# Kernel optimization log

Measured on AMD Instinct MI355X. Metric: run time of the kernel, lower is better.

Reference implementation:

```python
import jax, jax.numpy as jnp
import numpy as np

EPS_NORM = 1e-6  # MVLayerNorm epsilon


def _build_cayley():
    # Cl(3,0): blades as bitmasks, ordered by (grade, bitmask):
    # [1, e1, e2, e3, e12, e13, e23, e123]
    n = 3
    order = sorted(range(1 << n), key=lambda b: (bin(b).count('1'), b))
    idx = {b: i for i, b in enumerate(order)}
    C = np.zeros((8, 8, 8), dtype=np.float32)
    for a in range(8):
        for b in range(8):
            # sign from reordering basis vectors (Euclidean metric: e_i^2 = +1)
            swaps, ash = 0, a >> 1
            while ash:
                swaps += bin(ash & b).count('1')
                ash >>= 1
            C[idx[a], idx[a ^ b], idx[b]] = -1.0 if swaps % 2 else 1.0
    return C

_CAYLEY_NP = _build_cayley()
CAYLEY = jnp.asarray(_CAYLEY_NP)
# metric of each blade: scalar part of blade*blade -> [1,1,1,1,-1,-1,-1,-1]
METRIC = jnp.asarray(np.array([_CAYLEY_NP[i, 0, i] for i in range(8)], dtype=np.float32))
# blade -> grade subspace index, subspace dims [1,3,3,1]
BLADE2SUB = np.array([0, 1, 1, 1, 2, 2, 2, 3])


def mv_linear(x, w, b):
    # x: (B, in, 8); w: (out, in, 4); b: (out,) added to scalar blade only
    wb = w[:, :, BLADE2SUB]                      # (out, in, 8) per-blade weight
    y = jnp.einsum('bmi,nmi->bni', x, wb)        # (B, out, 8)
    return y.at[..., 0].add(b)


def mv_layernorm(x, a):
    # quadratic form per channel: q = sum_i g_i * x_i^2, shape (B, C, 1)
    q = jnp.einsum('bci,i,bci->bc', x, METRIC, x)[..., None]
    norm = (q * q + 1e-16) ** 0.25               # smooth sqrt(|q|)
    norm = norm.mean(axis=1, keepdims=True) + EPS_NORM  # (B, 1, 1)
    return a[None, :, None] * x / norm


def setup_inputs() -> dict:
    key = jax.random.key(0)
    ks = jax.random.split(key, 8)
    N, C_IN, C_HID, NSUB = 4096, 512, 512, 4
    s = 1.0 / np.sqrt(C_IN)
    return {
        'x': jax.random.normal(ks[0], (N, C_IN, 8), jnp.float32),
        'w1': jax.random.normal(ks[1], (C_HID, C_IN, NSUB), jnp.float32) * s,
        'b1': jax.random.normal(ks[2], (C_HID,), jnp.float32) * 0.02,
        'w2': jax.random.normal(ks[3], (C_HID, C_IN, NSUB), jnp.float32) * s,
        'b2': jax.random.normal(ks[4], (C_HID,), jnp.float32) * 0.02,
        'w3': jax.random.normal(ks[5], (C_IN, C_HID, NSUB), jnp.float32) * s,
        'b3': jax.random.normal(ks[6], (C_IN,), jnp.float32) * 0.02,
        'a_norm': jax.random.normal(ks[7], (C_IN,), jnp.float32) * 0.1 + 1.0,
    }


def reference(x, w1, b1, w2, b2, w3, b3, a_norm):
    x_l = mv_linear(x, w1, b1)                       # (N, hid, 8)
    x_r = mv_linear(x, w2, b2)                       # (N, hid, 8)
    gp = jnp.einsum('bni,ijk,bnk->bnj', x_l, CAYLEY, x_r)  # sparse Cayley product
    y = mv_linear(gp, w3, b3)                        # (N, in, 8)
    return mv_layernorm(y, a_norm)
```

## Files before the change

kernel.cpp:

```cpp
#include <hip/hip_runtime.h>
#include <hip/hip_bf16.h>
#include <cstdint>
#include <cstddef>

typedef __bf16 bf16;
typedef __bf16 bf16x2_t __attribute__((ext_vector_type(2)));
typedef __bf16 bf16x4_t __attribute__((ext_vector_type(4)));
typedef __bf16 bf16x8_t __attribute__((ext_vector_type(8)));
typedef float  f32x2_t  __attribute__((ext_vector_type(2)));
typedef float  f32x4_t  __attribute__((ext_vector_type(4)));
typedef unsigned int u32x4_t __attribute__((ext_vector_type(4)));

#define NTOK 4096
#define CH   512
#define SLICE (NTOK*CH)
#define WSLICE (CH*CH)

#define AS1 __attribute__((address_space(1)))
#define AS3 __attribute__((address_space(3)))

__device__ __forceinline__ void gl_lds16(const void* g, void* l) {
    __builtin_amdgcn_global_load_lds((const AS1 unsigned int*)g,
                                     (AS3 unsigned int*)l, 16, 0, 0);
}

__global__ __launch_bounds__(256) void k_convert_x(const float* __restrict__ x,
                                                   bf16* __restrict__ xb) {
    int p = blockIdx.x * 256 + threadIdx.x;
    const f32x4_t* x4 = (const f32x4_t*)x;
    f32x4_t v0 = x4[2*p];
    f32x4_t v1 = x4[2*p+1];
    xb[0*SLICE + p] = (bf16)v0.x;
    xb[1*SLICE + p] = (bf16)v0.y;
    xb[2*SLICE + p] = (bf16)v0.z;
    xb[3*SLICE + p] = (bf16)v0.w;
    xb[4*SLICE + p] = (bf16)v1.x;
    xb[5*SLICE + p] = (bf16)v1.y;
    xb[6*SLICE + p] = (bf16)v1.z;
    xb[7*SLICE + p] = (bf16)v1.w;
}

__global__ __launch_bounds__(256) void k_convert_w(const float* __restrict__ w1,
                                                   const float* __restrict__ w2,
                                                   const float* __restrict__ w3,
                                                   bf16* __restrict__ w1b,
                                                   bf16* __restrict__ w2b,
                                                   bf16* __restrict__ w3b) {
    int p = blockIdx.x * 256 + threadIdx.x;
    const float* w = (blockIdx.y == 0) ? w1 : (blockIdx.y == 1) ? w2 : w3;
    bf16* wb       = (blockIdx.y == 0) ? w1b : (blockIdx.y == 1) ? w2b : w3b;
    f32x4_t v = ((const f32x4_t*)w)[p];
    wb[0*WSLICE + p] = (bf16)v.x;
    wb[1*WSLICE + p] = (bf16)v.y;
    wb[2*WSLICE + p] = (bf16)v.z;
    wb[3*WSLICE + p] = (bf16)v.w;
}

template<int DUAL>
__global__ __launch_bounds__(256, 2) void k_gemm(const bf16* __restrict__ Abase,
                                                 const bf16* __restrict__ W1base,
                                                 const bf16* __restrict__ W2base,
                                                 bf16* __restrict__ O1base,
                                                 bf16* __restrict__ O2base) {
    const int blade = blockIdx.z;
    const int sub = (blade == 0) ? 0 : (blade < 4) ? 1 : (blade < 7) ? 2 : 3;
    const bf16* A  = Abase + (size_t)blade * SLICE;
    const bf16* B1 = W1base + (size_t)sub * WSLICE;
    const bf16* B2 = W2base + (size_t)sub * WSLICE;
    const int tm = blockIdx.x * 128, tn = blockIdx.y * 128;

    __shared__ __align__(1024) bf16 lsA[128 * 64];
    __shared__ __align__(1024) bf16 lsB1[128 * 64];
    __shared__ __align__(1024) bf16 lsB2[DUAL ? 128 * 64 : 64];
    char* lsAc  = (char*)lsA;
    char* lsB1c = (char*)lsB1;
    char* lsB2c = (char*)lsB2;

    const int t = threadIdx.x, lane = t & 63, wid = t >> 6;
    const int waveM = (wid >> 1) * 64, waveN = (wid & 1) * 64;

    const int srow = wid * 32 + (lane >> 3);
    const int sswz = ((lane & 7) ^ (srow & 7)) * 8;
    const bf16* Ag  = A  + (size_t)(tm + srow) * CH + sswz;
    const bf16* B1g = B1 + (size_t)(tn + srow) * CH + sswz;
    const bf16* B2g = B2 + (size_t)(tn + srow) * CH + sswz;
    const int ldsq = wid * 4096;

    const int xorv  = (lane & 7) << 4;
    const int kbase = (lane >> 4) * 16;

    f32x4_t accL[4][4] = {};
    f32x4_t accR[4][4] = {};

    #pragma unroll 1
    for (int kt = 0; kt < 8; ++kt) {
        __syncthreads();
        const int k0 = kt * 64;
        #pragma unroll
        for (int q = 0; q < 4; ++q) {
            gl_lds16(Ag  + (size_t)q * 8 * CH + k0, lsAc  + ldsq + q * 1024);
            gl_lds16(B1g + (size_t)q * 8 * CH + k0, lsB1c + ldsq + q * 1024);
            if constexpr (DUAL)
                gl_lds16(B2g + (size_t)q * 8 * CH + k0, lsB2c + ldsq + q * 1024);
        }
        __syncthreads();
        #pragma unroll
        for (int kk = 0; kk < 2; ++kk) {
            const int koff = kk * 64 + kbase;
            bf16x8_t af[4], b1v[4], b2v[4];
            #pragma unroll
            for (int mf = 0; mf < 4; ++mf) {
                int row = waveM + mf * 16 + (lane & 15);
                af[mf] = *(const bf16x8_t*)(lsAc + row * 128 + (koff ^ xorv));
            }
            #pragma unroll
            for (int nf = 0; nf < 4; ++nf) {
                int row = waveN + nf * 16 + (lane & 15);
                b1v[nf] = *(const bf16x8_t*)(lsB1c + row * 128 + (koff ^ xorv));
                if constexpr (DUAL)
                    b2v[nf] = *(const bf16x8_t*)(lsB2c + row * 128 + (koff ^ xorv));
            }
            #pragma unroll
            for (int mf = 0; mf < 4; ++mf)
                #pragma unroll
                for (int nf = 0; nf < 4; ++nf) {
                    accL[mf][nf] = __builtin_amdgcn_mfma_f32_16x16x32_bf16(
                        af[mf], b1v[nf], accL[mf][nf], 0, 0, 0);
                    if constexpr (DUAL)
                        accR[mf][nf] = __builtin_amdgcn_mfma_f32_16x16x32_bf16(
                            af[mf], b2v[nf], accR[mf][nf], 0, 0, 0);
                }
        }
    }

    const int orow0 = tm + waveM + (lane >> 4) * 4;
    const int ocol  = tn + waveN + (lane & 15);
    bf16* O1 = O1base + (size_t)blade * SLICE;
    #pragma unroll
    for (int mf = 0; mf < 4; ++mf)
        #pragma unroll
        for (int r = 0; r < 4; ++r) {
            size_t rowoff = (size_t)(orow0 + mf * 16 + r) * CH;
            #pragma unroll
            for (int nf = 0; nf < 4; ++nf)
                O1[rowoff + ocol + nf * 16] = (bf16)accL[mf][nf][r];
        }
    if constexpr (DUAL) {
        bf16* O2 = O2base + (size_t)blade * SLICE;
        #pragma unroll
        for (int mf = 0; mf < 4; ++mf)
            #pragma unroll
            for (int r = 0; r < 4; ++r) {
                size_t rowoff = (size_t)(orow0 + mf * 16 + r) * CH;
                #pragma unroll
                for (int nf = 0; nf < 4; ++nf)
                    O2[rowoff + ocol + nf * 16] = (bf16)accR[mf][nf][r];
            }
    }
}

__global__ __launch_bounds__(256) void k_gp(const bf16* __restrict__ xl,
                                            const bf16* __restrict__ xr,
                                            const float* __restrict__ b1,
                                            const float* __restrict__ b2,
                                            bf16* __restrict__ gp) {
    int p = (blockIdx.x * 256 + threadIdx.x) * 4;
    float l[8][4], r[8][4], g[8][4];
    #pragma unroll
    for (int i = 0; i < 8; ++i) {
        bf16x4_t lv = *(const bf16x4_t*)(xl + (size_t)i * SLICE + p);
        bf16x4_t rv = *(const bf16x4_t*)(xr + (size_t)i * SLICE + p);
        #pragma unroll
        for (int v = 0; v < 4; ++v) { l[i][v] = (float)lv[v]; r[i][v] = (float)rv[v]; g[i][v] = 0.f; }
    }
    int n0 = p & (CH - 1);
    f32x4_t b1v = *(const f32x4_t*)(b1 + n0);
    f32x4_t b2v = *(const f32x4_t*)(b2 + n0);
    #pragma unroll
    for (int v = 0; v < 4; ++v) { l[0][v] += b1v[v]; r[0][v] += b2v[v]; }

    const int IDX[8] = {0, 1, 2, 4, 3, 5, 6, 7};
    #pragma unroll
    for (int a = 0; a < 8; ++a) {
        #pragma unroll
        for (int b = 0; b < 8; ++b) {
            int e = ((((a >> 1) ^ (a >> 2)) & b) & 1) ^ (((a >> 2) & (b >> 1)) & 1);
            int j = IDX[a ^ b], ia = IDX[a], ib = IDX[b];
            #pragma unroll
            for (int v = 0; v < 4; ++v)
                g[j][v] += e ? (-l[ia][v] * r[ib][v]) : (l[ia][v] * r[ib][v]);
        }
    }
    #pragma unroll
    for (int i = 0; i < 8; ++i) {
        bf16x4_t gv;
        #pragma unroll
        for (int v = 0; v < 4; ++v) gv[v] = (bf16)g[i][v];
        *(bf16x4_t*)(gp + (size_t)i * SLICE + p) = gv;
    }
}

__global__ __launch_bounds__(256) void k_ln(const bf16* __restrict__ y,
                                            const float* __restrict__ b3,
                                            const float* __restrict__ an,
                                            float* __restrict__ out) {
    int b = blockIdx.x, t = threadIdx.x;
    int c0 = t * 2;
    size_t base = (size_t)b * CH + c0;
    float yv[2][8];
    #pragma unroll
    for (int i = 0; i < 8; ++i) {
        bf16x2_t v = *(const bf16x2_t*)(y + (size_t)i * SLICE + base);
        yv[0][i] = (float)v[0];
        yv[1][i] = (float)v[1];
    }
    f32x2_t b3v = *(const f32x2_t*)(b3 + c0);
    float nsum = 0.f;
    #pragma unroll
    for (int h = 0; h < 2; ++h) {
        yv[h][0] += b3v[h];
        float q = yv[h][0]*yv[h][0] + yv[h][1]*yv[h][1] + yv[h][2]*yv[h][2] + yv[h][3]*yv[h][3]
                - yv[h][4]*yv[h][4] - yv[h][5]*yv[h][5] - yv[h][6]*yv[h][6] - yv[h][7]*yv[h][7];
        nsum += sqrtf(sqrtf(q * q + 1e-16f));
    }
    #pragma unroll
    for (int off = 32; off; off >>= 1) nsum += __shfl_xor(nsum, off);
    __shared__ float red[4];
    if ((t & 63) == 0) red[t >> 6] = nsum;
    __syncthreads();
    float denom = (red[0] + red[1] + red[2] + red[3]) * (1.f / 512.f) + 1e-6f;
    float inv = 1.f / denom;
    f32x2_t anv = *(const f32x2_t*)(an + c0);
    float out16[16];
    #pragma unroll
    for (int h = 0; h < 2; ++h) {
        float s = anv[h] * inv;
        #pragma unroll
        for (int i = 0; i < 8; ++i) out16[h * 8 + i] = yv[h][i] * s;
    }
    size_t base8 = base * 8;
    #pragma unroll
    for (int j = 0; j < 4; ++j)
        *(f32x4_t*)(out + base8 + j * 4) = *(f32x4_t*)(out16 + j * 4);
}

extern "C" void kernel_launch(void* const* d_in, const int* in_sizes, int n_in,
                              void* d_out, int out_size, void* d_ws, size_t ws_size,
                              hipStream_t stream) {
    (void)in_sizes; (void)n_in; (void)out_size; (void)ws_size;
    const float* x  = (const float*)d_in[0];
    const float* w1 = (const float*)d_in[1];
    const float* b1 = (const float*)d_in[2];
    const float* w2 = (const float*)d_in[3];
    const float* b2 = (const float*)d_in[4];
    const float* w3 = (const float*)d_in[5];
    const float* b3 = (const float*)d_in[6];
    const float* an = (const float*)d_in[7];

    char* ws = (char*)d_ws;
    bf16*  xb  = (bf16*)(ws);
    bf16*  xl  = (bf16*)(ws + 33554432);
    bf16*  xr  = (bf16*)(ws + 67108864);
    bf16*  yb  = (bf16*)(ws + 33554432);
    bf16*  w1b = (bf16*)(ws + 100663296);
    bf16*  w2b = (bf16*)(ws + 102760448);
    bf16*  w3b = (bf16*)(ws + 104857600);

    k_convert_x<<<SLICE / 256, 256, 0, stream>>>(x, xb);
    dim3 gw(WSLICE / 256, 3);
    k_convert_w<<<gw, 256, 0, stream>>>(w1, w2, w3, w1b, w2b, w3b);

    dim3 gg(NTOK / 128, CH / 128, 8);
    k_gemm<1><<<gg, 256, 0, stream>>>(xb, w1b, w2b, xl, xr);
    k_gp<<<SLICE / 4 / 256, 256, 0, stream>>>(xl, xr, b1, b2, xb );
    k_gemm<0><<<gg, 256, 0, stream>>>(xb, w3b, w3b, yb, yb);
    k_ln<<<NTOK, 256, 0, stream>>>(yb, b3, an, (float*)d_out);
}
```

Before: 244.6 us.

## Double-buffer LDS and enlarge GEMM tiles with 512-thread blocks

Splits the templated GEMM into two kernels: a dual GEMM for the two input projections and a single GEMM for the output projection. Both now use 512-thread blocks with larger output tiles (256x128 and 256x256) and double-buffered LDS. The next K tile is prefetched through global_load_lds while the current one is multiplied, which halves the barriers per iteration. MFMA sections are wrapped in s_setprio. The aim is to hide global-load latency and raise data reuse per LDS byte. In exchange, each block now needs 128KB of LDS, which likely limits occupancy to one block per CU, and the GEMM3 grid shrinks to a single wave of blocks.

```diff
diff --git a/kernel.cpp b/kernel.cpp
--- a/kernel.cpp
+++ b/kernel.cpp
@@ -9,7 +9,6 @@
 typedef __bf16 bf16x8_t __attribute__((ext_vector_type(8)));
 typedef float  f32x2_t  __attribute__((ext_vector_type(2)));
 typedef float  f32x4_t  __attribute__((ext_vector_type(4)));
-typedef unsigned int u32x4_t __attribute__((ext_vector_type(4)));
 
 #define NTOK 4096
 #define CH   512
@@ -56,107 +55,208 @@
     wb[3*WSLICE + p] = (bf16)v.w;
 }
 
-template<int DUAL>
-__global__ __launch_bounds__(256, 2) void k_gemm(const bf16* __restrict__ Abase,
-                                                 const bf16* __restrict__ W1base,
-                                                 const bf16* __restrict__ W2base,
-                                                 bf16* __restrict__ O1base,
-                                                 bf16* __restrict__ O2base) {
+__global__ __launch_bounds__(512, 2) void k_gemm12(const bf16* __restrict__ xb,
+                                                   const bf16* __restrict__ w1b,
+                                                   const bf16* __restrict__ w2b,
+                                                   bf16* __restrict__ xl,
+                                                   bf16* __restrict__ xr) {
     const int blade = blockIdx.z;
     const int sub = (blade == 0) ? 0 : (blade < 4) ? 1 : (blade < 7) ? 2 : 3;
-    const bf16* A  = Abase + (size_t)blade * SLICE;
-    const bf16* B1 = W1base + (size_t)sub * WSLICE;
-    const bf16* B2 = W2base + (size_t)sub * WSLICE;
-    const int tm = blockIdx.x * 128, tn = blockIdx.y * 128;
-
-    __shared__ __align__(1024) bf16 lsA[128 * 64];
-    __shared__ __align__(1024) bf16 lsB1[128 * 64];
-    __shared__ __align__(1024) bf16 lsB2[DUAL ? 128 * 64 : 64];
-    char* lsAc  = (char*)lsA;
-    char* lsB1c = (char*)lsB1;
-    char* lsB2c = (char*)lsB2;
+    const bf16* A  = xb  + (size_t)blade * SLICE;
+    const bf16* B1 = w1b + (size_t)sub * WSLICE;
+    const bf16* B2 = w2b + (size_t)sub * WSLICE;
+    const int tm = blockIdx.x * 256, tn = blockIdx.y * 128;
+
+    __shared__ __align__(1024) bf16 lsA[2][256 * 64];
+    __shared__ __align__(1024) bf16 lsB1[2][128 * 64];
+    __shared__ __align__(1024) bf16 lsB2[2][128 * 64];
 
     const int t = threadIdx.x, lane = t & 63, wid = t >> 6;
-    const int waveM = (wid >> 1) * 64, waveN = (wid & 1) * 64;
-
-    const int srow = wid * 32 + (lane >> 3);
-    const int sswz = ((lane & 7) ^ (srow & 7)) * 8;
+    const int waveM = (wid >> 2) * 128, waveN = (wid & 3) * 32;
+
+    const int srow = t >> 3;
+    const int sswz = ((t & 7) ^ (srow & 7)) * 8;
     const bf16* Ag  = A  + (size_t)(tm + srow) * CH + sswz;
     const bf16* B1g = B1 + (size_t)(tn + srow) * CH + sswz;
     const bf16* B2g = B2 + (size_t)(tn + srow) * CH + sswz;
-    const int ldsq = wid * 4096;
+    const int wbase = wid * 1024;
 
     const int xorv  = (lane & 7) << 4;
     const int kbase = (lane >> 4) * 16;
 
-    f32x4_t accL[4][4] = {};
-    f32x4_t accR[4][4] = {};
-
-    #pragma unroll 1
+    f32x4_t accL[8][2] = {};
+    f32x4_t accR[8][2] = {};
+
+    {
+        char* la  = (char*)lsA[0]  + wbase;
+        char* lb1 = (char*)lsB1[0] + wbase;
+        char* lb2 = (char*)lsB2[0] + wbase;
+        #pragma unroll
+        for (int q = 0; q < 4; ++q)
+            gl_lds16(Ag + (size_t)q * 64 * CH, la + q * 8192);
+        #pragma unroll
+        for (int q = 0; q < 2; ++q) {
+            gl_lds16(B1g + (size_t)q * 64 * CH, lb1 + q * 8192);
+            gl_lds16(B2g + (size_t)q * 64 * CH, lb2 + q * 8192);
+        }
+    }
+
+    #pragma unroll 2
     for (int kt = 0; kt < 8; ++kt) {
+        const int cur = kt & 1;
         __syncthreads();
-        const int k0 = kt * 64;
-        #pragma unroll
-        for (int q = 0; q < 4; ++q) {
-            gl_lds16(Ag  + (size_t)q * 8 * CH + k0, lsAc  + ldsq + q * 1024);
-            gl_lds16(B1g + (size_t)q * 8 * CH + k0, lsB1c + ldsq + q * 1024);
-            if constexpr (DUAL)
-                gl_lds16(B2g + (size_t)q * 8 * CH + k0, lsB2c + ldsq + q * 1024);
-        }
-        __syncthreads();
+        if (kt < 7) {
+            const int k0 = (kt + 1) * 64;
+            char* la  = (char*)lsA[cur ^ 1]  + wbase;
+            char* lb1 = (char*)lsB1[cur ^ 1] + wbase;
+            char* lb2 = (char*)lsB2[cur ^ 1] + wbase;
+            #pragma unroll
+            for (int q = 0; q < 4; ++q)
+                gl_lds16(Ag + (size_t)q * 64 * CH + k0, la + q * 8192);
+            #pragma unroll
+            for (int q = 0; q < 2; ++q) {
+                gl_lds16(B1g + (size_t)q * 64 * CH + k0, lb1 + q * 8192);
+                gl_lds16(B2g + (size_t)q * 64 * CH + k0, lb2 + q * 8192);
+            }
+        }
+        const char* ca  = (const char*)lsA[cur];
+        const char* cb1 = (const char*)lsB1[cur];
+        const char* cb2 = (const char*)lsB2[cur];
         #pragma unroll
         for (int kk = 0; kk < 2; ++kk) {
             const int koff = kk * 64 + kbase;
-            bf16x8_t af[4], b1v[4], b2v[4];
-            #pragma unroll
-            for (int mf = 0; mf < 4; ++mf) {
+            bf16x8_t af[8], b1f[2], b2f[2];
+            #pragma unroll
+            for (int mf = 0; mf < 8; ++mf) {
                 int row = waveM + mf * 16 + (lane & 15);
-                af[mf] = *(const bf16x8_t*)(lsAc + row * 128 + (koff ^ xorv));
+                af[mf] = *(const bf16x8_t*)(ca + row * 128 + (koff ^ xorv));
+            }
+            #pragma unroll
+            for (int nf = 0; nf < 2; ++nf) {
+                int row = waveN + nf * 16 + (lane & 15);
+                b1f[nf] = *(const bf16x8_t*)(cb1 + row * 128 + (koff ^ xorv));
+                b2f[nf] = *(const bf16x8_t*)(cb2 + row * 128 + (koff ^ xorv));
+            }
+            __builtin_amdgcn_s_setprio(1);
+            #pragma unroll
+            for (int mf = 0; mf < 8; ++mf)
+                #pragma unroll
+                for (int nf = 0; nf < 2; ++nf) {
+                    accL[mf][nf] = __builtin_amdgcn_mfma_f32_16x16x32_bf16(
+                        af[mf], b1f[nf], accL[mf][nf], 0, 0, 0);
+                    accR[mf][nf] = __builtin_amdgcn_mfma_f32_16x16x32_bf16(
+                        af[mf], b2f[nf], accR[mf][nf], 0, 0, 0);
+                }
+            __builtin_amdgcn_s_setprio(0);
+        }
+    }
+
+    bf16* O1 = xl + (size_t)blade * SLICE;
+    bf16* O2 = xr + (size_t)blade * SLICE;
+    const int orow0 = tm + waveM + (lane >> 4) * 4;
+    const int ocol  = tn + waveN + (lane & 15);
+    #pragma unroll
+    for (int mf = 0; mf < 8; ++mf)
+        #pragma unroll
+        for (int r = 0; r < 4; ++r) {
+            size_t rowoff = (size_t)(orow0 + mf * 16 + r) * CH;
+            #pragma unroll
+            for (int nf = 0; nf < 2; ++nf) {
+                O1[rowoff + ocol + nf * 16] = (bf16)accL[mf][nf][r];
+                O2[rowoff + ocol + nf * 16] = (bf16)accR[mf][nf][r];
+            }
+        }
+}
+
+__global__ __launch_bounds__(512, 2) void k_gemm3(const bf16* __restrict__ gp,
+                                                  const bf16* __restrict__ w3b,
+                                                  bf16* __restrict__ yb) {
+    const int blade = blockIdx.z;
+    const int sub = (blade == 0) ? 0 : (blade < 4) ? 1 : (blade < 7) ? 2 : 3;
+    const bf16* A = gp  + (size_t)blade * SLICE;
+    const bf16* B = w3b + (size_t)sub * WSLICE;
+    const int tm = blockIdx.x * 256, tn = blockIdx.y * 256;
+
+    __shared__ __align__(1024) bf16 lsA[2][256 * 64];
+    __shared__ __align__(1024) bf16 lsB[2][256 * 64];
+
+    const int t = threadIdx.x, lane = t & 63, wid = t >> 6;
+    const int waveM = (wid >> 2) * 128, waveN = (wid & 3) * 64;
+
+    const int srow = t >> 3;
+    const int sswz = ((t & 7) ^ (srow & 7)) * 8;
+    const bf16* Ag = A + (size_t)(tm + srow) * CH + sswz;
+    const bf16* Bg = B + (size_t)(tn + srow) * CH + sswz;
+    const int wbase = wid * 1024;
+
+    const int xorv  = (lane & 7) << 4;
+    const int kbase = (lane >> 4) * 16;
+
+    f32x4_t acc[8][4] = {};
+
+    {
+        char* la = (char*)lsA[0] + wbase;
+        char* lb = (char*)lsB[0] + wbase;
+        #pragma unroll
+        for (int q = 0; q < 4; ++q) {
+            gl_lds16(Ag + (size_t)q * 64 * CH, la + q * 8192);
+            gl_lds16(Bg + (size_t)q * 64 * CH, lb + q * 8192);
+        }
+    }
+
+    #pragma unroll 2
+    for (int kt = 0; kt < 8; ++kt) {
+        const int cur = kt & 1;
+        __syncthreads();
+        if (kt < 7) {
+            const int k0 = (kt + 1) * 64;
+            char* la = (char*)lsA[cur ^ 1] + wbase;
+            char* lb = (char*)lsB[cur ^ 1] + wbase;
+            #pragma unroll
+            for (int q = 0; q < 4; ++q) {
+                gl_lds16(Ag + (size_t)q * 64 * CH + k0, la + q * 8192);
+                gl_lds16(Bg + (size_t)q * 64 * CH + k0, lb + q * 8192);
+            }
+        }
+        const char* ca = (const char*)lsA[cur];
+        const char* cb = (const char*)lsB[cur];
+        #pragma unroll
+        for (int kk = 0; kk < 2; ++kk) {
+            const int koff = kk * 64 + kbase;
+            bf16x8_t af[8], bf[4];
+            #pragma unroll
+            for (int mf = 0; mf < 8; ++mf) {
+                int row = waveM + mf * 16 + (lane & 15);
+                af[mf] = *(const bf16x8_t*)(ca + row * 128 + (koff ^ xorv));
             }
             #pragma unroll
             for (int nf = 0; nf < 4; ++nf) {
                 int row = waveN + nf * 16 + (lane & 15);
-                b1v[nf] = *(const bf16x8_t*)(lsB1c + row * 128 + (koff ^ xorv));
-                if constexpr (DUAL)
-                    b2v[nf] = *(const bf16x8_t*)(lsB2c + row * 128 + (koff ^ xorv));
-            }
-            #pragma unroll
-            for (int mf = 0; mf < 4; ++mf)
+                bf[nf] = *(const bf16x8_t*)(cb + row * 128 + (koff ^ xorv));
+            }
+            __builtin_amdgcn_s_setprio(1);
+            #pragma unroll
+            for (int mf = 0; mf < 8; ++mf)
                 #pragma unroll
-                for (int nf = 0; nf < 4; ++nf) {
-                    accL[mf][nf] = __builtin_amdgcn_mfma_f32_16x16x32_bf16(
-                        af[mf], b1v[nf], accL[mf][nf], 0, 0, 0);
-                    if constexpr (DUAL)
-                        accR[mf][nf] = __builtin_amdgcn_mfma_f32_16x16x32_bf16(
-                            af[mf], b2v[nf], accR[mf][nf], 0, 0, 0);
-                }
-        }
-    }
-
+                for (int nf = 0; nf < 4; ++nf)
+                    acc[mf][nf] = __builtin_amdgcn_mfma_f32_16x16x32_bf16(
+                        af[mf], bf[nf], acc[mf][nf], 0, 0, 0);
+            __builtin_amdgcn_s_setprio(0);
+        }
+    }
+
+    bf16* O = yb + (size_t)blade * SLICE;
     const int orow0 = tm + waveM + (lane >> 4) * 4;
     const int ocol  = tn + waveN + (lane & 15);
-    bf16* O1 = O1base + (size_t)blade * SLICE;
-    #pragma unroll
-    for (int mf = 0; mf < 4; ++mf)
+    #pragma unroll
+    for (int mf = 0; mf < 8; ++mf)
         #pragma unroll
         for (int r = 0; r < 4; ++r) {
             size_t rowoff = (size_t)(orow0 + mf * 16 + r) * CH;
             #pragma unroll
             for (int nf = 0; nf < 4; ++nf)
-                O1[rowoff + ocol + nf * 16] = (bf16)accL[mf][nf][r];
-        }
-    if constexpr (DUAL) {
-        bf16* O2 = O2base + (size_t)blade * SLICE;
-        #pragma unroll
-        for (int mf = 0; mf < 4; ++mf)
-            #pragma unroll
-            for (int r = 0; r < 4; ++r) {
-                size_t rowoff = (size_t)(orow0 + mf * 16 + r) * CH;
-                #pragma unroll
-                for (int nf = 0; nf < 4; ++nf)
-                    O2[rowoff + ocol + nf * 16] = (bf16)accR[mf][nf][r];
-            }
-    }
+                O[rowoff + ocol + nf * 16] = (bf16)acc[mf][nf][r];
+        }
 }
 
 __global__ __launch_bounds__(256) void k_gp(const bf16* __restrict__ xl,
@@ -270,9 +370,10 @@
     dim3 gw(WSLICE / 256, 3);
     k_convert_w<<<gw, 256, 0, stream>>>(w1, w2, w3, w1b, w2b, w3b);
 
-    dim3 gg(NTOK / 128, CH / 128, 8);
-    k_gemm<1><<<gg, 256, 0, stream>>>(xb, w1b, w2b, xl, xr);
+    dim3 g12(NTOK / 256, CH / 128, 8);
+    k_gemm12<<<g12, 512, 0, stream>>>(xb, w1b, w2b, xl, xr);
     k_gp<<<SLICE / 4 / 256, 256, 0, stream>>>(xl, xr, b1, b2, xb );
-    k_gemm<0><<<gg, 256, 0, stream>>>(xb, w3b, w3b, yb, yb);
+    dim3 g3(NTOK / 256, CH / 256, 8);
+    k_gemm3<<<g3, 512, 0, stream>>>(xb, w3b, yb);
     k_ln<<<NTOK, 256, 0, stream>>>(yb, b3, an, (float*)d_out);
 }
```

Result: no change. 246.4 us (+0.7%).

## Load weight fragments directly from global and swap MFMA operands for vector stores

Applied to the files above, without the earlier changes.

Stops staging the weight tiles in LDS. Each wave now reads its B fragments straight from global memory (expected to hit L2, since the weights are small), and only the activation tile goes through LDS. The MFMA operands are swapped so the accumulator layout lets each lane write four contiguous bf16 outputs as a single vector store instead of scalar stores. The templated GEMM is split into separate dual and single kernels. The trade-off is more global load latency inside the inner loop with no LDS reuse of B across waves, in exchange for less LDS traffic, fewer barriers' worth of data and lower LDS footprint.

```diff
diff --git a/kernel.cpp b/kernel.cpp
--- a/kernel.cpp
+++ b/kernel.cpp
@@ -9,7 +9,6 @@
 typedef __bf16 bf16x8_t __attribute__((ext_vector_type(8)));
 typedef float  f32x2_t  __attribute__((ext_vector_type(2)));
 typedef float  f32x4_t  __attribute__((ext_vector_type(4)));
-typedef unsigned int u32x4_t __attribute__((ext_vector_type(4)));
 
 #define NTOK 4096
 #define CH   512
@@ -56,58 +55,51 @@
     wb[3*WSLICE + p] = (bf16)v.w;
 }
 
-template<int DUAL>
-__global__ __launch_bounds__(256, 2) void k_gemm(const bf16* __restrict__ Abase,
-                                                 const bf16* __restrict__ W1base,
-                                                 const bf16* __restrict__ W2base,
-                                                 bf16* __restrict__ O1base,
-                                                 bf16* __restrict__ O2base) {
+__global__ __launch_bounds__(256, 2) void k_gemm12(const bf16* __restrict__ xb,
+                                                   const bf16* __restrict__ w1b,
+                                                   const bf16* __restrict__ w2b,
+                                                   bf16* __restrict__ xl,
+                                                   bf16* __restrict__ xr) {
     const int blade = blockIdx.z;
     const int sub = (blade == 0) ? 0 : (blade < 4) ? 1 : (blade < 7) ? 2 : 3;
-    const bf16* A  = Abase + (size_t)blade * SLICE;
-    const bf16* B1 = W1base + (size_t)sub * WSLICE;
-    const bf16* B2 = W2base + (size_t)sub * WSLICE;
+    const bf16* A  = xb  + (size_t)blade * SLICE;
+    const bf16* B1 = w1b + (size_t)sub * WSLICE;
+    const bf16* B2 = w2b + (size_t)sub * WSLICE;
     const int tm = blockIdx.x * 128, tn = blockIdx.y * 128;
 
     __shared__ __align__(1024) bf16 lsA[128 * 64];
-    __shared__ __align__(1024) bf16 lsB1[128 * 64];
-    __shared__ __align__(1024) bf16 lsB2[DUAL ? 128 * 64 : 64];
-    char* lsAc  = (char*)lsA;
-    char* lsB1c = (char*)lsB1;
-    char* lsB2c = (char*)lsB2;
+    char* lsAc = (char*)lsA;
 
     const int t = threadIdx.x, lane = t & 63, wid = t >> 6;
     const int waveM = (wid >> 1) * 64, waveN = (wid & 1) * 64;
 
     const int srow = wid * 32 + (lane >> 3);
-    const int sswz = ((lane & 7) ^ (srow & 7)) * 8;
-    const bf16* Ag  = A  + (size_t)(tm + srow) * CH + sswz;
-    const bf16* B1g = B1 + (size_t)(tn + srow) * CH + sswz;
-    const bf16* B2g = B2 + (size_t)(tn + srow) * CH + sswz;
+    const int sswz = ((lane & 7) ^ (lane >> 3)) * 8;
+    const bf16* Ag = A + (size_t)(tm + srow) * CH + sswz;
     const int ldsq = wid * 4096;
 
     const int xorv  = (lane & 7) << 4;
     const int kbase = (lane >> 4) * 16;
 
+    const bf16* B1t = B1 + (size_t)(tn + waveN + (lane & 15)) * CH + (lane >> 4) * 8;
+    const bf16* B2t = B2 + (size_t)(tn + waveN + (lane & 15)) * CH + (lane >> 4) * 8;
+
     f32x4_t accL[4][4] = {};
     f32x4_t accR[4][4] = {};
 
     #pragma unroll 1
     for (int kt = 0; kt < 8; ++kt) {
+        const int k0 = kt * 64;
         __syncthreads();
-        const int k0 = kt * 64;
-        #pragma unroll
-        for (int q = 0; q < 4; ++q) {
-            gl_lds16(Ag  + (size_t)q * 8 * CH + k0, lsAc  + ldsq + q * 1024);
-            gl_lds16(B1g + (size_t)q * 8 * CH + k0, lsB1c + ldsq + q * 1024);
-            if constexpr (DUAL)
-                gl_lds16(B2g + (size_t)q * 8 * CH + k0, lsB2c + ldsq + q * 1024);
-        }
+        #pragma unroll
+        for (int q = 0; q < 4; ++q)
+            gl_lds16(Ag + (size_t)q * 8 * CH + k0, lsAc + ldsq + q * 1024);
         __syncthreads();
         #pragma unroll
         for (int kk = 0; kk < 2; ++kk) {
             const int koff = kk * 64 + kbase;
-            bf16x8_t af[4], b1v[4], b2v[4];
+            const int gk   = k0 + kk * 32;
+            bf16x8_t af[4], b1f[4], b2f[4];
             #pragma unroll
             for (int mf = 0; mf < 4; ++mf) {
                 int row = waveM + mf * 16 + (lane & 15);
@@ -115,47 +107,110 @@
             }
             #pragma unroll
             for (int nf = 0; nf < 4; ++nf) {
-                int row = waveN + nf * 16 + (lane & 15);
-                b1v[nf] = *(const bf16x8_t*)(lsB1c + row * 128 + (koff ^ xorv));
-                if constexpr (DUAL)
-                    b2v[nf] = *(const bf16x8_t*)(lsB2c + row * 128 + (koff ^ xorv));
+                b1f[nf] = *(const bf16x8_t*)(B1t + (size_t)nf * 16 * CH + gk);
+                b2f[nf] = *(const bf16x8_t*)(B2t + (size_t)nf * 16 * CH + gk);
             }
             #pragma unroll
             for (int mf = 0; mf < 4; ++mf)
                 #pragma unroll
                 for (int nf = 0; nf < 4; ++nf) {
                     accL[mf][nf] = __builtin_amdgcn_mfma_f32_16x16x32_bf16(
-                        af[mf], b1v[nf], accL[mf][nf], 0, 0, 0);
-                    if constexpr (DUAL)
-                        accR[mf][nf] = __builtin_amdgcn_mfma_f32_16x16x32_bf16(
-                            af[mf], b2v[nf], accR[mf][nf], 0, 0, 0);
+                        b1f[nf], af[mf], accL[mf][nf], 0, 0, 0);
+                    accR[mf][nf] = __builtin_amdgcn_mfma_f32_16x16x32_bf16(
+                        b2f[nf], af[mf], accR[mf][nf], 0, 0, 0);
                 }
         }
     }
 
-    const int orow0 = tm + waveM + (lane >> 4) * 4;
-    const int ocol  = tn + waveN + (lane & 15);
-    bf16* O1 = O1base + (size_t)blade * SLICE;
-    #pragma unroll
-    for (int mf = 0; mf < 4; ++mf)
-        #pragma unroll
-        for (int r = 0; r < 4; ++r) {
-            size_t rowoff = (size_t)(orow0 + mf * 16 + r) * CH;
+    bf16* O1 = xl + (size_t)blade * SLICE;
+    bf16* O2 = xr + (size_t)blade * SLICE;
+    #pragma unroll
+    for (int mf = 0; mf < 4; ++mf) {
+        size_t rowoff = (size_t)(tm + waveM + mf * 16 + (lane & 15)) * CH;
+        #pragma unroll
+        for (int nf = 0; nf < 4; ++nf) {
+            int ch = tn + waveN + nf * 16 + (lane >> 4) * 4;
+            bf16x4_t v1, v2;
+            #pragma unroll
+            for (int r = 0; r < 4; ++r) {
+                v1[r] = (bf16)accL[mf][nf][r];
+                v2[r] = (bf16)accR[mf][nf][r];
+            }
+            *(bf16x4_t*)(O1 + rowoff + ch) = v1;
+            *(bf16x4_t*)(O2 + rowoff + ch) = v2;
+        }
+    }
+}
+
+__global__ __launch_bounds__(256, 2) void k_gemm3(const bf16* __restrict__ gp,
+                                                  const bf16* __restrict__ w3b,
+                                                  bf16* __restrict__ yb) {
+    const int blade = blockIdx.z;
+    const int sub = (blade == 0) ? 0 : (blade < 4) ? 1 : (blade < 7) ? 2 : 3;
+    const bf16* A = gp  + (size_t)blade * SLICE;
+    const bf16* B = w3b + (size_t)sub * WSLICE;
+    const int tm = blockIdx.x * 128, tn = blockIdx.y * 128;
+
+    __shared__ __align__(1024) bf16 lsA[128 * 64];
+    char* lsAc = (char*)lsA;
+
+    const int t = threadIdx.x, lane = t & 63, wid = t >> 6;
+    const int waveM = (wid >> 1) * 64, waveN = (wid & 1) * 64;
+
+    const int srow = wid * 32 + (lane >> 3);
+    const int sswz = ((lane & 7) ^ (lane >> 3)) * 8;
+    const bf16* Ag = A + (size_t)(tm + srow) * CH + sswz;
+    const int ldsq = wid * 4096;
+
+    const int xorv  = (lane & 7) << 4;
+    const int kbase = (lane >> 4) * 16;
+
+    const bf16* Bt = B + (size_t)(tn + waveN + (lane & 15)) * CH + (lane >> 4) * 8;
+
+    f32x4_t acc[4][4] = {};
+
+    #pragma unroll 1
+    for (int kt = 0; kt < 8; ++kt) {
+        const int k0 = kt * 64;
+        __syncthreads();
+        #pragma unroll
+        for (int q = 0; q < 4; ++q)
+            gl_lds16(Ag + (size_t)q * 8 * CH + k0, lsAc + ldsq + q * 1024);
+        __syncthreads();
+        #pragma unroll
+        for (int kk = 0; kk < 2; ++kk) {
+            const int koff = kk * 64 + kbase;
+            const int gk   = k0 + kk * 32;
+            bf16x8_t af[4], bf[4];
+            #pragma unroll
+            for (int mf = 0; mf < 4; ++mf) {
+                int row = waveM + mf * 16 + (lane & 15);
+                af[mf] = *(const bf16x8_t*)(lsAc + row * 128 + (koff ^ xorv));
+            }
             #pragma unroll
             for (int nf = 0; nf < 4; ++nf)
-                O1[rowoff + ocol + nf * 16] = (bf16)accL[mf][nf][r];
-        }
-    if constexpr (DUAL) {
-        bf16* O2 = O2base + (size_t)blade * SLICE;
-        #pragma unroll
-        for (int mf = 0; mf < 4; ++mf)
-            #pragma unroll
-            for (int r = 0; r < 4; ++r) {
-                size_t rowoff = (size_t)(orow0 + mf * 16 + r) * CH;
+                bf[nf] = *(const bf16x8_t*)(Bt + (size_t)nf * 16 * CH + gk);
+            #pragma unroll
+            for (int mf = 0; mf < 4; ++mf)
                 #pragma unroll
                 for (int nf = 0; nf < 4; ++nf)
-                    O2[rowoff + ocol + nf * 16] = (bf16)accR[mf][nf][r];
-            }
+                    acc[mf][nf] = __builtin_amdgcn_mfma_f32_16x16x32_bf16(
+                        bf[nf], af[mf], acc[mf][nf], 0, 0, 0);
+        }
+    }
+
+    bf16* O = yb + (size_t)blade * SLICE;
+    #pragma unroll
+    for (int mf = 0; mf < 4; ++mf) {
+        size_t rowoff = (size_t)(tm + waveM + mf * 16 + (lane & 15)) * CH;
+        #pragma unroll
+        for (int nf = 0; nf < 4; ++nf) {
+            int ch = tn + waveN + nf * 16 + (lane >> 4) * 4;
+            bf16x4_t v;
+            #pragma unroll
+            for (int r = 0; r < 4; ++r) v[r] = (bf16)acc[mf][nf][r];
+            *(bf16x4_t*)(O + rowoff + ch) = v;
+        }
     }
 }
 
@@ -271,8 +326,8 @@
     k_convert_w<<<gw, 256, 0, stream>>>(w1, w2, w3, w1b, w2b, w3b);
 
     dim3 gg(NTOK / 128, CH / 128, 8);
-    k_gemm<1><<<gg, 256, 0, stream>>>(xb, w1b, w2b, xl, xr);
+    k_gemm12<<<gg, 256, 0, stream>>>(xb, w1b, w2b, xl, xr);
     k_gp<<<SLICE / 4 / 256, 256, 0, stream>>>(xl, xr, b1, b2, xb );
-    k_gemm<0><<<gg, 256, 0, stream>>>(xb, w3b, w3b, yb, yb);
+    k_gemm3<<<gg, 256, 0, stream>>>(xb, w3b, yb);
     k_ln<<<NTOK, 256, 0, stream>>>(yb, b3, an, (float*)d_out);
 }
```

After: 305.4 us. 1.25x slower.
